# Kernel optimization log

Measured on AMD Instinct MI355X. Metric: run time of the kernel, lower is better.

Reference implementation:

```python
import jax, jax.numpy as jnp
import numpy as np

B, F = 512, 300  # F must satisfy F+4 == 16*19
EPS = 1e-5

def _leaky(v):
    return jnp.where(v >= 0, v, 0.01 * v)

def setup_inputs() -> dict:
    key = jax.random.key(0)
    ks = jax.random.split(key, 9)
    def conv_w(k, o, i):
        return jax.random.normal(k, (o, i), dtype=jnp.float32) * (1.0 / np.sqrt(i))
    x = jax.random.uniform(ks[0], (B, F), dtype=jnp.float32)
    return {
        "x": x,
        "w1": conv_w(ks[1], 256, 512), "b1": jnp.zeros((256,), jnp.float32),
        "w2": conv_w(ks[2], 128, 256), "b2": jnp.zeros((128,), jnp.float32),
        "w3": conv_w(ks[3], 64, 128),  "b3": jnp.zeros((64,), jnp.float32),
        "w4": conv_w(ks[4], 4, 64),    "b4": jnp.zeros((4,), jnp.float32),
    }

def reference(x, w1, b1, w2, b2, w3, b3, w4, b4):
    b = x.shape[0]
    xp = jnp.pad(x, ((0, 0), (2, 2)))                       # (b, 304)
    s1 = xp[:, None, :]                                      # unsqueeze(1)
    s2 = xp[:, :, None]                                      # unsqueeze(2)
    DI = s1 - s2                                             # (b,304,304)
    NDI = DI / (s1 + s2 + EPS)
    t = jnp.stack([DI, NDI], axis=-1)                        # (b,304,304,2)
    # tile into 16x16 grid of 19x19 patches, concat patches along channel
    # channel c = (row*16+col)*2 + d  (row-major loop order in original)
    t = t.reshape(b, 16, 19, 16, 19, 2).transpose(0, 2, 4, 1, 3, 5).reshape(b, 19, 19, 512)
    h = _leaky(jnp.einsum('bhwc,oc->bhwo', t, w1) + b1)      # (b,19,19,256)
    h = _leaky(jnp.einsum('bhwc,oc->bhwo', h, w2) + b2)      # (b,19,19,128)
    # masking branch (positional encoding in original is dead code / overwritten)
    m = jax.nn.relu(jnp.einsum('bhwc,oc->bhwo', h, w3) + b3)  # (b,19,19,64)
    m = jax.nn.relu(jnp.einsum('bhwc,oc->bhwo', m, w4) + b4)  # (b,19,19,4)
    m = m.transpose(3, 0, 1, 2).reshape(4, b, 19 * 19)
    m = jax.nn.softmax(m, axis=2).reshape(4, b, 19, 19, 1)
    # split 128 channels into 4 groups of 32
    g = h.reshape(b, 19, 19, 4, 32).transpose(3, 0, 1, 2, 4)  # (4,b,19,19,32)
    out = (g * m).sum(axis=(2, 3))                            # (4,b,32)
    return out.transpose(1, 0, 2).reshape(b, 128)
```

## Files before the change

### kernel.cpp

```cpp
#include <hip/hip_runtime.h>
#include <math.h>

typedef unsigned short ushort_t;
typedef __attribute__((ext_vector_type(8))) short short8;
typedef __attribute__((ext_vector_type(4))) float f32x4;

#define NTILES 12

#define WS_W_USHORTS 114688

__device__ inline ushort_t f2bf(float f) {
    unsigned u = __float_as_uint(f);
    return (ushort_t)((u + 0x7FFFu + ((u >> 16) & 1u)) >> 16);
}
__device__ inline unsigned pkbf(float f0, float f1) {
    unsigned a = __float_as_uint(f0) + 0x8000u;
    unsigned b = __float_as_uint(f1) + 0x8000u;
    return __builtin_amdgcn_perm(b, a, 0x07060302u);
}
__device__ inline float leaky(float v) { return fmaxf(v, 0.01f * v); }

__global__ void pack_weights(const float* __restrict__ w1, const float* __restrict__ w2,
                             const float* __restrict__ w3, ushort_t* __restrict__ ws) {
    const int idx = blockIdx.x * 256 + threadIdx.x;
    if (idx >= WS_W_USHORTS) return;
    float val = 0.f;
    if (idx < 73728) {
        const int j = idx & 7, lane = (idx >> 3) & 63, blk = idx >> 9;
        const int ks = blk % 9, os = blk / 9;
        const int m = lane & 15, q = lane >> 4;
        const int row = os * 16 + m;
        if (ks < 8) {
            const int k = ks * 32 + q * 8 + j;
            const int i1 = k >> 4, j1 = k & 15;
            val = w1[row * 512 + i1 * 32 + j1 * 2 + 1];
        } else {
            const int sub = q * 8 + j;
            if (sub < 16) {
                const int j1 = sub;
                float s = 0.f;
                #pragma unroll
                for (int i1 = 0; i1 < 16; ++i1) s += w1[row * 512 + i1 * 32 + j1 * 2];
                val = s;
            } else {
                const int i1 = sub - 16;
                float s = 0.f;
                #pragma unroll
                for (int j1 = 0; j1 < 16; ++j1) s += w1[row * 512 + i1 * 32 + j1 * 2];
                val = -s;
            }
        }
    } else if (idx < 106496) {
        const int l = idx - 73728;
        const int j = l & 7, lane = (l >> 3) & 63, blk = l >> 9;
        const int ks = blk & 7, os = blk >> 3;
        const int m = lane & 15, q = lane >> 4;
        val = w2[(os * 16 + m) * 256 + ks * 32 + q * 8 + j];
    } else {
        const int l = idx - 106496;
        const int j = l & 7, lane = (l >> 3) & 63, blk = l >> 9;
        const int ks = blk & 3, os = blk >> 2;
        const int m = lane & 15, q = lane >> 4;
        val = w3[(os * 16 + m) * 128 + ks * 32 + q * 8 + j];
    }
    ws[idx] = f2bf(val);
}

template <int NS>
__global__ __launch_bounds__(256, 3) void fused_mfma(
    const float* __restrict__ x, const ushort_t* __restrict__ ws,
    const float* __restrict__ b1, const float* __restrict__ b2,
    const float* __restrict__ b3, const float* __restrict__ b4,
    const float* __restrict__ w4,
    float* __restrict__ partA, float* __restrict__ partS)
{
    __shared__ __align__(16) ushort_t sm[19048];
    ushort_t* const ts   = sm;
    ushort_t* const h2s  = sm;
    ushort_t* const h1s  = sm + 10240;
    float*   const wbuf  = (float*)(sm + 10240);
    float*   const xp    = (float*)(sm + 18432);

    constexpr int SH  = (NS == 4) ? 2 : ((NS == 2) ? 1 : 0);
    constexpr int TPS = (NTILES + NS - 1) / NS;
    const int tid = threadIdx.x;
    const int s   = blockIdx.x & (NS - 1);
    const int bb  = blockIdx.x >> SH;
    const int t0  = s * TPS;
    const int t1  = (t0 + TPS < NTILES) ? (t0 + TPS) : NTILES;

    const int wid  = tid >> 6;
    const int lane = tid & 63;
    const int n0   = lane & 15;
    const int qi   = lane >> 4;
    const int sx   = n0 & 7;
    const int row0 = qi * 4;

    for (int jj = tid; jj < 308; jj += 256) {
        float v = 0.f;
        const int src = jj - 2;
        if (src >= 0 && src < 300) v = x[bb * 300 + src];
        xp[jj] = v;
    }

    const short8* wf1 = (const short8*)(ws);
    const short8* wf2 = (const short8*)(ws + 73728);
    const short8* wf3 = (const short8*)(ws + 106496);

    f32x4 bv1[4], bv2[2], bv3;
    #pragma unroll
    for (int jo = 0; jo < 4; ++jo) bv1[jo] = *(const f32x4*)&b1[(wid * 4 + jo) * 16 + row0];
    #pragma unroll
    for (int jo = 0; jo < 2; ++jo) bv2[jo] = *(const f32x4*)&b2[(wid * 2 + jo) * 16 + row0];
    bv3 = *(const f32x4*)&b3[wid * 16 + row0];
    short8 wr3[4];
    #pragma unroll
    for (int ks = 0; ks < 4; ++ks) wr3[ks] = wf3[(wid * 4 + ks) * 64 + lane];
    f32x4 w4r[4];
    #pragma unroll
    for (int q = 0; q < 4; ++q) w4r[q] = *(const f32x4*)&w4[q * 64 + wid * 16 + row0];
    const float b4s = b4[wid];

    f32x4 Afr[2] = {{0.f, 0.f, 0.f, 0.f}, {0.f, 0.f, 0.f, 0.f}};
    float Ss = 0.f;

    __syncthreads();

    for (int tile = t0; tile < t1; ++tile) {
        const int pos0 = tile * 32;

        {
            const int p   = tid & 31;
            const int i1b = tid >> 5;
            int posg = pos0 + p; if (posg > 360) posg = 360;
            const int hh = posg / 19;
            const int ww = posg - 19 * hh;
            const int base = p * 320;
            const int psw  = p & 7;
            float u[16];
            #pragma unroll
            for (int j1 = 0; j1 < 16; ++j1) u[j1] = xp[j1 * 19 + ww];
            #pragma unroll
            for (int ii = 0; ii < 2; ++ii) {
                const int i1 = i1b + ii * 8;
                const float v = xp[i1 * 19 + hh];
                #pragma unroll
                for (int j1 = 0; j1 < 16; j1 += 2) {
                    const float nd0 = (u[j1] - v)     * __builtin_amdgcn_rcpf(u[j1] + v + 1e-5f);
                    const float nd1 = (u[j1 + 1] - v) * __builtin_amdgcn_rcpf(u[j1 + 1] + v + 1e-5f);
                    const int oct = i1 * 2 + (j1 >> 3);
                    *(unsigned*)&ts[base + ((oct ^ psw) << 3) + (j1 & 7)] = pkbf(nd0, nd1);
                }
            }
            if (i1b == 0) {
                #pragma unroll
                for (int j1 = 0; j1 < 16; j1 += 2) {
                    const int oct = 32 + (j1 >> 3);
                    *(unsigned*)&ts[base + ((oct ^ psw) << 3) + (j1 & 7)] = pkbf(u[j1], u[j1 + 1]);
                }
                #pragma unroll
                for (int i1 = 0; i1 < 16; i1 += 2) {
                    const float v0 = xp[i1 * 19 + hh];
                    const float v1 = xp[(i1 + 1) * 19 + hh];
                    const int oct = 34 + (i1 >> 3);
                    *(unsigned*)&ts[base + ((oct ^ psw) << 3) + (i1 & 7)] = pkbf(v0, v1);
                }
            }
        }
        __syncthreads();

        {
            f32x4 acc[4][2];
            #pragma unroll
            for (int jo = 0; jo < 4; ++jo) { acc[jo][0] = bv1[jo]; acc[jo][1] = bv1[jo]; }
            const int tb0 = n0 * 320;
            const int tb1 = tb0 + 16 * 320;
            const int wbase = wid * 2304 + lane;
            #pragma unroll 3
            for (int ks = 0; ks < 9; ++ks) {
                const int oct = ks * 4 + qi;
                const short8 bb0 = *(const short8*)&ts[tb0 + ((oct ^ sx) << 3)];
                const short8 bb1 = *(const short8*)&ts[tb1 + ((oct ^ sx) << 3)];
                #pragma unroll
                for (int jo = 0; jo < 4; ++jo) {
                    const short8 a = wf1[wbase + (jo * 9 + ks) * 64];
                    acc[jo][0] = __builtin_amdgcn_mfma_f32_16x16x32_bf16(a, bb0, acc[jo][0], 0, 0, 0);
                    acc[jo][1] = __builtin_amdgcn_mfma_f32_16x16x32_bf16(a, bb1, acc[jo][1], 0, 0, 0);
                }
            }
            #pragma unroll
            for (int jo = 0; jo < 4; ++jo) {
                const int out0 = (wid * 4 + jo) * 16 + row0;
                #pragma unroll
                for (int ps = 0; ps < 2; ++ps) {
                    const f32x4 a4 = acc[jo][ps];
                    uint2 pk;
                    pk.x = pkbf(leaky(a4.x), leaky(a4.y));
                    pk.y = pkbf(leaky(a4.z), leaky(a4.w));
                    *(uint2*)&h1s[(ps * 16 + n0) * 256 + (((out0 >> 3) ^ sx) << 3) + (out0 & 7)] = pk;
                }
            }
        }
        __syncthreads();

        f32x4 h2f[2][2];
        {
            f32x4 acc[2][2];
            #pragma unroll
            for (int jo = 0; jo < 2; ++jo) { acc[jo][0] = bv2[jo]; acc[jo][1] = bv2[jo]; }
            const int hb0 = n0 * 256;
            const int hb1 = hb0 + 16 * 256;
            const int wbase = wid * 1024 + lane;
            #pragma unroll 4
            for (int ks = 0; ks < 8; ++ks) {
                const int oct = ks * 4 + qi;
                const short8 bb0 = *(const short8*)&h1s[hb0 + ((oct ^ sx) << 3)];
                const short8 bb1 = *(const short8*)&h1s[hb1 + ((oct ^ sx) << 3)];
                #pragma unroll
                for (int jo = 0; jo < 2; ++jo) {
                    const short8 a = wf2[wbase + (jo * 8 + ks) * 64];
                    acc[jo][0] = __builtin_amdgcn_mfma_f32_16x16x32_bf16(a, bb0, acc[jo][0], 0, 0, 0);
                    acc[jo][1] = __builtin_amdgcn_mfma_f32_16x16x32_bf16(a, bb1, acc[jo][1], 0, 0, 0);
                }
            }
            #pragma unroll
            for (int jo = 0; jo < 2; ++jo) {
                const int out0 = (wid * 2 + jo) * 16 + row0;
                #pragma unroll
                for (int ps = 0; ps < 2; ++ps) {
                    f32x4 a4 = acc[jo][ps];
                    a4.x = leaky(a4.x); a4.y = leaky(a4.y);
                    a4.z = leaky(a4.z); a4.w = leaky(a4.w);
                    h2f[jo][ps] = a4;
                    uint2 pk;
                    pk.x = pkbf(a4.x, a4.y);
                    pk.y = pkbf(a4.z, a4.w);
                    *(uint2*)&h2s[(ps * 16 + n0) * 128 + (((out0 >> 3) ^ sx) << 3) + (out0 & 7)] = pk;
                }
            }
        }
        __syncthreads();

        {
            f32x4 acc[2] = {bv3, bv3};
            const int cb0 = n0 * 128;
            const int cb1 = cb0 + 16 * 128;
            #pragma unroll
            for (int ks = 0; ks < 4; ++ks) {
                const int oct = ks * 4 + qi;
                const short8 bb0 = *(const short8*)&h2s[cb0 + ((oct ^ sx) << 3)];
                const short8 bb1 = *(const short8*)&h2s[cb1 + ((oct ^ sx) << 3)];
                acc[0] = __builtin_amdgcn_mfma_f32_16x16x32_bf16(wr3[ks], bb0, acc[0], 0, 0, 0);
                acc[1] = __builtin_amdgcn_mfma_f32_16x16x32_bf16(wr3[ks], bb1, acc[1], 0, 0, 0);
            }
            #pragma unroll
            for (int ps = 0; ps < 2; ++ps) {
                f32x4 m3 = acc[ps];
                m3.x = fmaxf(m3.x, 0.f); m3.y = fmaxf(m3.y, 0.f);
                m3.z = fmaxf(m3.z, 0.f); m3.w = fmaxf(m3.w, 0.f);
                float pl[4];
                #pragma unroll
                for (int q = 0; q < 4; ++q)
                    pl[q] = w4r[q].x * m3.x + w4r[q].y * m3.y + w4r[q].z * m3.z + w4r[q].w * m3.w;
                #pragma unroll
                for (int q = 0; q < 4; ++q) {
                    pl[q] += __shfl_xor(pl[q], 16, 64);
                    pl[q] += __shfl_xor(pl[q], 32, 64);
                }
                if (qi == 0) {
                    #pragma unroll
                    for (int q = 0; q < 4; ++q)
                        wbuf[(wid * 4 + q) * 32 + ps * 16 + n0] = pl[q];
                }
            }
        }
        __syncthreads();

        {
            #pragma unroll
            for (int ps = 0; ps < 2; ++ps) {
                const int pos = ps * 16 + n0;
                float lg = wbuf[(0 * 4 + wid) * 32 + pos] + wbuf[(1 * 4 + wid) * 32 + pos]
                         + wbuf[(2 * 4 + wid) * 32 + pos] + wbuf[(3 * 4 + wid) * 32 + pos] + b4s;
                lg = fmaxf(lg, 0.f);
                const float e = ((pos0 + pos) > 360) ? 0.f : __expf(lg);
                #pragma unroll
                for (int jo = 0; jo < 2; ++jo) {
                    Afr[jo].x += e * h2f[jo][ps].x;
                    Afr[jo].y += e * h2f[jo][ps].y;
                    Afr[jo].z += e * h2f[jo][ps].z;
                    Afr[jo].w += e * h2f[jo][ps].w;
                }
                Ss += e;
            }
        }
    }

    #pragma unroll
    for (int bit = 1; bit < 16; bit <<= 1) {
        #pragma unroll
        for (int jo = 0; jo < 2; ++jo) {
            Afr[jo].x += __shfl_xor(Afr[jo].x, bit, 64);
            Afr[jo].y += __shfl_xor(Afr[jo].y, bit, 64);
            Afr[jo].z += __shfl_xor(Afr[jo].z, bit, 64);
            Afr[jo].w += __shfl_xor(Afr[jo].w, bit, 64);
        }
        Ss += __shfl_xor(Ss, bit, 64);
    }
    if (n0 == 0) {
        const int pbA = (s * 512 + bb) * 128;
        #pragma unroll
        for (int jo = 0; jo < 2; ++jo) {
            const int ch0 = (wid * 2 + jo) * 16 + qi * 4;
            partA[pbA + ch0]     = Afr[jo].x;
            partA[pbA + ch0 + 1] = Afr[jo].y;
            partA[pbA + ch0 + 2] = Afr[jo].z;
            partA[pbA + ch0 + 3] = Afr[jo].w;
        }
        if (qi == 0) partS[(s * 512 + bb) * 4 + wid] = Ss;
    }
}

template <int NS>
__global__ void merge_out(const float* __restrict__ partA, const float* __restrict__ partS,
                          float* __restrict__ out) {
    const int idx = blockIdx.x * 256 + threadIdx.x;
    if (idx >= 512 * 128) return;
    const int bb = idx >> 7, ch = idx & 127;
    const int q = ch >> 5;
    float Sf = 0.f, Af = 0.f;
    #pragma unroll
    for (int s = 0; s < NS; ++s) {
        Af += partA[(s * 512 + bb) * 128 + ch];
        Sf += partS[(s * 512 + bb) * 4 + q];
    }
    out[idx] = Af / Sf;
}

__global__ __launch_bounds__(256, 2) void fallback_fused(
    const float* __restrict__ x,
    const float* __restrict__ w1, const float* __restrict__ b1,
    const float* __restrict__ w2, const float* __restrict__ b2,
    const float* __restrict__ w3, const float* __restrict__ b3,
    const float* __restrict__ w4, const float* __restrict__ b4,
    float* __restrict__ out)
{
    __shared__ float smf[14644];
    float* const xp  = smf;
    float* const ts  = smf + 308;
    float* const h1s = smf + 8500;
    float* const h2s = smf + 12596;
    float* const m3s = ts;
    float* const lgs = ts + 1024;

    const int tid = threadIdx.x;
    const int b   = blockIdx.x;
    for (int j = tid; j < 308; j += 256) {
        float v = 0.f;
        const int src = j - 2;
        if (src >= 0 && src < 300) v = x[b * 300 + src];
        xp[j] = v;
    }
    __syncthreads();
    const int q = tid >> 5, dd = tid & 31;
    float M = -1e30f, S = 0.f, A = 0.f;
    for (int tile = 0; tile < 23; ++tile) {
        const int pos0 = tile * 16;
        {
            const int p = tid & 15, kk0 = tid >> 4;
            const int pos = pos0 + p;
            const bool valid = (pos < 361);
            const int hh = valid ? (pos / 19) : 0;
            const int ww = valid ? (pos - hh * 19) : 0;
            #pragma unroll
            for (int i = 0; i < 16; ++i) {
                const int kk = kk0 + (i << 4);
                const int i1 = kk >> 4, j1 = kk & 15;
                float di = 0.f, ndi = 0.f;
                if (valid) {
                    const float u = xp[j1 * 19 + ww];
                    const float v = xp[i1 * 19 + hh];
                    di = u - v; ndi = di / (u + v + 1e-5f);
                }
                ts[(kk << 5) + p] = di;
                ts[(kk << 5) + 16 + p] = ndi;
            }
        }
        __syncthreads();
        {
            const int o = tid;
            float acc[16];
            const float bias = b1[o];
            #pragma unroll
            for (int p = 0; p < 16; ++p) acc[p] = bias;
            for (int k = 0; k < 512; ++k) {
                const float wv = w1[o * 512 + k];
                #pragma unroll
                for (int p = 0; p < 16; ++p) acc[p] += wv * ts[(k << 4) + p];
            }
            #pragma unroll
            for (int p = 0; p < 16; ++p) h1s[(o << 4) + p] = (acc[p] >= 0.f) ? acc[p] : 0.01f * acc[p];
        }
        __syncthreads();
        {
            const int o2 = tid & 127, pb = (tid >> 7) << 3;
            float acc[8];
            const float bias = b2[o2];
            #pragma unroll
            for (int j = 0; j < 8; ++j) acc[j] = bias;
            for (int k = 0; k < 256; ++k) {
                const float wv = w2[o2 * 256 + k];
                #pragma unroll
                for (int j = 0; j < 8; ++j) acc[j] += wv * h1s[(k << 4) + pb + j];
            }
            #pragma unroll
            for (int j = 0; j < 8; ++j) h2s[(o2 << 4) + pb + j] = (acc[j] >= 0.f) ? acc[j] : 0.01f * acc[j];
        }
        __syncthreads();
        {
            const int o3 = tid & 63, pb = (tid >> 6) << 2;
            float acc[4];
            const float bias = b3[o3];
            #pragma unroll
            for (int j = 0; j < 4; ++j) acc[j] = bias;
            for (int k = 0; k < 128; ++k) {
                const float wv = w3[o3 * 128 + k];
                #pragma unroll
                for (int j = 0; j < 4; ++j) acc[j] += wv * h2s[(k << 4) + pb + j];
            }
            #pragma unroll
            for (int j = 0; j < 4; ++j) m3s[(o3 << 4) + pb + j] = fmaxf(acc[j], 0.f);
        }
        __syncthreads();
        if (tid < 64) {
            const int o4 = tid >> 4, p = tid & 15;
            float a = b4[o4];
            for (int k = 0; k < 64; ++k) a += w4[o4 * 64 + k] * m3s[(k << 4) + p];
            a = fmaxf(a, 0.f);
            if (pos0 + p >= 361) a = -1e30f;
            lgs[(o4 << 4) + p] = a;
        }
        __syncthreads();
        if (tid < 128) {
            float l[16];
            #pragma unroll
            for (int p = 0; p < 16; ++p) l[p] = lgs[(q << 4) + p];
            float tmax = l[0];
            #pragma unroll
            for (int p = 1; p < 16; ++p) tmax = fmaxf(tmax, l[p]);
            const float newM = fmaxf(M, tmax);
            const float alpha = __expf(M - newM);
            float ssum = 0.f, asum = 0.f;
            #pragma unroll
            for (int p = 0; p < 16; ++p) {
                const float e = __expf(l[p] - newM);
                ssum += e;
                asum += e * h2s[(((q << 5) + dd) << 4) + p];
            }
            S = S * alpha + ssum; A = A * alpha + asum; M = newM;
        }
        __syncthreads();
    }
    if (tid < 128) out[(b << 7) + tid] = A / S;
}

extern "C" void kernel_launch(void* const* d_in, const int* in_sizes, int n_in,
                              void* d_out, int out_size, void* d_ws, size_t ws_size,
                              hipStream_t stream) {
    const float* x  = (const float*)d_in[0];
    const float* w1 = (const float*)d_in[1];
    const float* b1 = (const float*)d_in[2];
    const float* w2 = (const float*)d_in[3];
    const float* b2 = (const float*)d_in[4];
    const float* w3 = (const float*)d_in[5];
    const float* b3 = (const float*)d_in[6];
    const float* w4 = (const float*)d_in[7];
    const float* b4 = (const float*)d_in[8];
    float* out = (float*)d_out;

    const size_t wbytes = (size_t)WS_W_USHORTS * sizeof(ushort_t);
    ushort_t* ws = (ushort_t*)d_ws;
    const int packBlocks = (WS_W_USHORTS + 255) / 256;

    const size_t need4 = wbytes + (size_t)4 * 512 * 132 * sizeof(float);
    const size_t need2 = wbytes + (size_t)2 * 512 * 132 * sizeof(float);
    const size_t need1 = wbytes + (size_t)1 * 512 * 132 * sizeof(float);

    if (ws_size >= need4) {
        float* pA = (float*)((char*)d_ws + wbytes);
        float* pS = pA + (size_t)4 * 512 * 128;
        pack_weights<<<packBlocks, 256, 0, stream>>>(w1, w2, w3, ws);
        fused_mfma<4><<<2048, 256, 0, stream>>>(x, ws, b1, b2, b3, b4, w4, pA, pS);
        merge_out<4><<<256, 256, 0, stream>>>(pA, pS, out);
    } else if (ws_size >= need2) {
        float* pA = (float*)((char*)d_ws + wbytes);
        float* pS = pA + (size_t)2 * 512 * 128;
        pack_weights<<<packBlocks, 256, 0, stream>>>(w1, w2, w3, ws);
        fused_mfma<2><<<1024, 256, 0, stream>>>(x, ws, b1, b2, b3, b4, w4, pA, pS);
        merge_out<2><<<256, 256, 0, stream>>>(pA, pS, out);
    } else if (ws_size >= need1) {
        float* pA = (float*)((char*)d_ws + wbytes);
        float* pS = pA + (size_t)1 * 512 * 128;
        pack_weights<<<packBlocks, 256, 0, stream>>>(w1, w2, w3, ws);
        fused_mfma<1><<<512, 256, 0, stream>>>(x, ws, b1, b2, b3, b4, w4, pA, pS);
        merge_out<1><<<256, 256, 0, stream>>>(pA, pS, out);
    } else {
        fallback_fused<<<512, 256, 0, stream>>>(x, w1, b1, w2, b2, w3, b3, w4, b4, out);
    }
}
```

Baseline: 168.7 us.

## Switch layer-1/2 GEMMs to 32x32x16 MFMA with matching weight packing

Repacks w1 and w2 into the 32x32x16 bf16 MFMA fragment layout and rewrites the first two pointwise GEMMs to use 32x32 tiles. Each wave now handles one 32-position tile, which halves the LDS B-fragment reads per MFMA and changes the accumulator layout to 16 floats. The LDS swizzle changes to (n + n/8)&7 to avoid bank conflicts for 32-row access. The softmax accumulation and cross-lane reduction follow the new layout. Layer-3 weights and w4 now load inside the tile loop rather than being held in registers, which lowers register pressure but adds repeated global loads.

```diff
diff --git a/kernel.cpp b/kernel.cpp
--- a/kernel.cpp
+++ b/kernel.cpp
@@ -4,6 +4,7 @@
 typedef unsigned short ushort_t;
 typedef __attribute__((ext_vector_type(8))) short short8;
 typedef __attribute__((ext_vector_type(4))) float f32x4;
+typedef __attribute__((ext_vector_type(16))) float f32x16;
 
 #define NTILES 12
 
@@ -27,15 +28,15 @@
     float val = 0.f;
     if (idx < 73728) {
         const int j = idx & 7, lane = (idx >> 3) & 63, blk = idx >> 9;
-        const int ks = blk % 9, os = blk / 9;
-        const int m = lane & 15, q = lane >> 4;
-        const int row = os * 16 + m;
-        if (ks < 8) {
-            const int k = ks * 32 + q * 8 + j;
+        const int ks = blk % 18, os = blk / 18;
+        const int m = lane & 31, hf = lane >> 5;
+        const int row = os * 32 + m;
+        const int k = ks * 16 + hf * 8 + j;
+        if (k < 256) {
             const int i1 = k >> 4, j1 = k & 15;
             val = w1[row * 512 + i1 * 32 + j1 * 2 + 1];
         } else {
-            const int sub = q * 8 + j;
+            const int sub = k - 256;
             if (sub < 16) {
                 const int j1 = sub;
                 float s = 0.f;
@@ -53,9 +54,9 @@
     } else if (idx < 106496) {
         const int l = idx - 73728;
         const int j = l & 7, lane = (l >> 3) & 63, blk = l >> 9;
-        const int ks = blk & 7, os = blk >> 3;
-        const int m = lane & 15, q = lane >> 4;
-        val = w2[(os * 16 + m) * 256 + ks * 32 + q * 8 + j];
+        const int ks = blk & 15, os = blk >> 4;
+        const int m = lane & 31, hf = lane >> 5;
+        val = w2[(os * 32 + m) * 256 + ks * 16 + hf * 8 + j];
     } else {
         const int l = idx - 106496;
         const int j = l & 7, lane = (l >> 3) & 63, blk = l >> 9;
@@ -89,12 +90,16 @@
     const int t0  = s * TPS;
     const int t1  = (t0 + TPS < NTILES) ? (t0 + TPS) : NTILES;
 
-    const int wid  = tid >> 6;
-    const int lane = tid & 63;
-    const int n0   = lane & 15;
-    const int qi   = lane >> 4;
-    const int sx   = n0 & 7;
-    const int row0 = qi * 4;
+    const int wid   = tid >> 6;
+    const int lane  = tid & 63;
+    const int n     = lane & 31;
+    const int half5 = lane >> 5;
+    const int sxn   = (n + (n >> 3)) & 7;
+    const int n0  = lane & 15;
+    const int qi  = lane >> 4;
+    const int sxa = (n0 + (n0 >> 3)) & 7;
+    const int n0b = n0 + 16;
+    const int sxb = (n0b + (n0b >> 3)) & 7;
 
     for (int jj = tid; jj < 308; jj += 256) {
         float v = 0.f;
@@ -107,21 +112,26 @@
     const short8* wf2 = (const short8*)(ws + 73728);
     const short8* wf3 = (const short8*)(ws + 106496);
 
-    f32x4 bv1[4], bv2[2], bv3;
+    f32x16 bv1f[2], bv2f;
     #pragma unroll
-    for (int jo = 0; jo < 4; ++jo) bv1[jo] = *(const f32x4*)&b1[(wid * 4 + jo) * 16 + row0];
+    for (int jo = 0; jo < 2; ++jo) {
+        #pragma unroll
+        for (int g = 0; g < 4; ++g) {
+            const f32x4 t4 = *(const f32x4*)&b1[(wid * 2 + jo) * 32 + 8 * g + 4 * half5];
+            bv1f[jo][4 * g + 0] = t4.x; bv1f[jo][4 * g + 1] = t4.y;
+            bv1f[jo][4 * g + 2] = t4.z; bv1f[jo][4 * g + 3] = t4.w;
+        }
+    }
     #pragma unroll
-    for (int jo = 0; jo < 2; ++jo) bv2[jo] = *(const f32x4*)&b2[(wid * 2 + jo) * 16 + row0];
-    bv3 = *(const f32x4*)&b3[wid * 16 + row0];
-    short8 wr3[4];
-    #pragma unroll
-    for (int ks = 0; ks < 4; ++ks) wr3[ks] = wf3[(wid * 4 + ks) * 64 + lane];
-    f32x4 w4r[4];
-    #pragma unroll
-    for (int q = 0; q < 4; ++q) w4r[q] = *(const f32x4*)&w4[q * 64 + wid * 16 + row0];
+    for (int g = 0; g < 4; ++g) {
+        const f32x4 t4 = *(const f32x4*)&b2[wid * 32 + 8 * g + 4 * half5];
+        bv2f[4 * g + 0] = t4.x; bv2f[4 * g + 1] = t4.y;
+        bv2f[4 * g + 2] = t4.z; bv2f[4 * g + 3] = t4.w;
+    }
+    const f32x4 bv3 = *(const f32x4*)&b3[wid * 16 + qi * 4];
     const float b4s = b4[wid];
 
-    f32x4 Afr[2] = {{0.f, 0.f, 0.f, 0.f}, {0.f, 0.f, 0.f, 0.f}};
+    f32x16 Afr = {0.f};
     float Ss = 0.f;
 
     __syncthreads();
@@ -136,7 +146,7 @@
             const int hh = posg / 19;
             const int ww = posg - 19 * hh;
             const int base = p * 320;
-            const int psw  = p & 7;
+            const int sxp  = (p + (p >> 3)) & 7;
             float u[16];
             #pragma unroll
             for (int j1 = 0; j1 < 16; ++j1) u[j1] = xp[j1 * 19 + ww];
@@ -149,113 +159,96 @@
                     const float nd0 = (u[j1] - v)     * __builtin_amdgcn_rcpf(u[j1] + v + 1e-5f);
                     const float nd1 = (u[j1 + 1] - v) * __builtin_amdgcn_rcpf(u[j1 + 1] + v + 1e-5f);
                     const int oct = i1 * 2 + (j1 >> 3);
-                    *(unsigned*)&ts[base + ((oct ^ psw) << 3) + (j1 & 7)] = pkbf(nd0, nd1);
+                    *(unsigned*)&ts[base + ((oct ^ sxp) << 3) + (j1 & 7)] = pkbf(nd0, nd1);
                 }
             }
             if (i1b == 0) {
                 #pragma unroll
                 for (int j1 = 0; j1 < 16; j1 += 2) {
                     const int oct = 32 + (j1 >> 3);
-                    *(unsigned*)&ts[base + ((oct ^ psw) << 3) + (j1 & 7)] = pkbf(u[j1], u[j1 + 1]);
+                    *(unsigned*)&ts[base + ((oct ^ sxp) << 3) + (j1 & 7)] = pkbf(u[j1], u[j1 + 1]);
                 }
                 #pragma unroll
                 for (int i1 = 0; i1 < 16; i1 += 2) {
                     const float v0 = xp[i1 * 19 + hh];
                     const float v1 = xp[(i1 + 1) * 19 + hh];
                     const int oct = 34 + (i1 >> 3);
-                    *(unsigned*)&ts[base + ((oct ^ psw) << 3) + (i1 & 7)] = pkbf(v0, v1);
-                }
-            }
-        }
-        __syncthreads();
-
-        {
-            f32x4 acc[4][2];
-            #pragma unroll
-            for (int jo = 0; jo < 4; ++jo) { acc[jo][0] = bv1[jo]; acc[jo][1] = bv1[jo]; }
-            const int tb0 = n0 * 320;
-            const int tb1 = tb0 + 16 * 320;
-            const int wbase = wid * 2304 + lane;
-            #pragma unroll 3
-            for (int ks = 0; ks < 9; ++ks) {
-                const int oct = ks * 4 + qi;
-                const short8 bb0 = *(const short8*)&ts[tb0 + ((oct ^ sx) << 3)];
-                const short8 bb1 = *(const short8*)&ts[tb1 + ((oct ^ sx) << 3)];
-                #pragma unroll
-                for (int jo = 0; jo < 4; ++jo) {
-                    const short8 a = wf1[wbase + (jo * 9 + ks) * 64];
-                    acc[jo][0] = __builtin_amdgcn_mfma_f32_16x16x32_bf16(a, bb0, acc[jo][0], 0, 0, 0);
-                    acc[jo][1] = __builtin_amdgcn_mfma_f32_16x16x32_bf16(a, bb1, acc[jo][1], 0, 0, 0);
-                }
-            }
-            #pragma unroll
-            for (int jo = 0; jo < 4; ++jo) {
-                const int out0 = (wid * 4 + jo) * 16 + row0;
-                #pragma unroll
-                for (int ps = 0; ps < 2; ++ps) {
-                    const f32x4 a4 = acc[jo][ps];
+                    *(unsigned*)&ts[base + ((oct ^ sxp) << 3) + (i1 & 7)] = pkbf(v0, v1);
+                }
+            }
+        }
+        __syncthreads();
+
+        {
+            f32x16 acc[2] = {bv1f[0], bv1f[1]};
+            const int tb = n * 320;
+            #pragma unroll 6
+            for (int ks = 0; ks < 18; ++ks) {
+                const int oct = ks * 2 + half5;
+                const short8 bbv = *(const short8*)&ts[tb + ((oct ^ sxn) << 3)];
+                acc[0] = __builtin_amdgcn_mfma_f32_32x32x16_bf16(
+                    wf1[((wid * 2 + 0) * 18 + ks) * 64 + lane], bbv, acc[0], 0, 0, 0);
+                acc[1] = __builtin_amdgcn_mfma_f32_32x32x16_bf16(
+                    wf1[((wid * 2 + 1) * 18 + ks) * 64 + lane], bbv, acc[1], 0, 0, 0);
+            }
+            #pragma unroll
+            for (int jo = 0; jo < 2; ++jo) {
+                const int osb = (wid * 2 + jo) * 32;
+                #pragma unroll
+                for (int g = 0; g < 4; ++g) {
                     uint2 pk;
-                    pk.x = pkbf(leaky(a4.x), leaky(a4.y));
-                    pk.y = pkbf(leaky(a4.z), leaky(a4.w));
-                    *(uint2*)&h1s[(ps * 16 + n0) * 256 + (((out0 >> 3) ^ sx) << 3) + (out0 & 7)] = pk;
-                }
-            }
-        }
-        __syncthreads();
-
-        f32x4 h2f[2][2];
-        {
-            f32x4 acc[2][2];
-            #pragma unroll
-            for (int jo = 0; jo < 2; ++jo) { acc[jo][0] = bv2[jo]; acc[jo][1] = bv2[jo]; }
-            const int hb0 = n0 * 256;
-            const int hb1 = hb0 + 16 * 256;
-            const int wbase = wid * 1024 + lane;
-            #pragma unroll 4
-            for (int ks = 0; ks < 8; ++ks) {
-                const int oct = ks * 4 + qi;
-                const short8 bb0 = *(const short8*)&h1s[hb0 + ((oct ^ sx) << 3)];
-                const short8 bb1 = *(const short8*)&h1s[hb1 + ((oct ^ sx) << 3)];
-                #pragma unroll
-                for (int jo = 0; jo < 2; ++jo) {
-                    const short8 a = wf2[wbase + (jo * 8 + ks) * 64];
-                    acc[jo][0] = __builtin_amdgcn_mfma_f32_16x16x32_bf16(a, bb0, acc[jo][0], 0, 0, 0);
-                    acc[jo][1] = __builtin_amdgcn_mfma_f32_16x16x32_bf16(a, bb1, acc[jo][1], 0, 0, 0);
-                }
-            }
-            #pragma unroll
-            for (int jo = 0; jo < 2; ++jo) {
-                const int out0 = (wid * 2 + jo) * 16 + row0;
-                #pragma unroll
-                for (int ps = 0; ps < 2; ++ps) {
-                    f32x4 a4 = acc[jo][ps];
-                    a4.x = leaky(a4.x); a4.y = leaky(a4.y);
-                    a4.z = leaky(a4.z); a4.w = leaky(a4.w);
-                    h2f[jo][ps] = a4;
-                    uint2 pk;
-                    pk.x = pkbf(a4.x, a4.y);
-                    pk.y = pkbf(a4.z, a4.w);
-                    *(uint2*)&h2s[(ps * 16 + n0) * 128 + (((out0 >> 3) ^ sx) << 3) + (out0 & 7)] = pk;
-                }
-            }
-        }
-        __syncthreads();
-
-        {
-            f32x4 acc[2] = {bv3, bv3};
+                    pk.x = pkbf(leaky(acc[jo][4 * g + 0]), leaky(acc[jo][4 * g + 1]));
+                    pk.y = pkbf(leaky(acc[jo][4 * g + 2]), leaky(acc[jo][4 * g + 3]));
+                    const int ch0 = osb + 8 * g + 4 * half5;
+                    *(uint2*)&h1s[n * 256 + (((ch0 >> 3) ^ sxn) << 3) + (ch0 & 7)] = pk;
+                }
+            }
+        }
+        __syncthreads();
+
+        f32x16 h2v;
+        {
+            f32x16 acc = bv2f;
+            const int hb = n * 256;
+            #pragma unroll 8
+            for (int ks = 0; ks < 16; ++ks) {
+                const int oct = ks * 2 + half5;
+                const short8 bbv = *(const short8*)&h1s[hb + ((oct ^ sxn) << 3)];
+                acc = __builtin_amdgcn_mfma_f32_32x32x16_bf16(
+                    wf2[(wid * 16 + ks) * 64 + lane], bbv, acc, 0, 0, 0);
+            }
+            #pragma unroll
+            for (int r = 0; r < 16; ++r) h2v[r] = leaky(acc[r]);
+            #pragma unroll
+            for (int g = 0; g < 4; ++g) {
+                uint2 pk;
+                pk.x = pkbf(h2v[4 * g + 0], h2v[4 * g + 1]);
+                pk.y = pkbf(h2v[4 * g + 2], h2v[4 * g + 3]);
+                const int ch0 = wid * 32 + 8 * g + 4 * half5;
+                *(uint2*)&h2s[n * 128 + (((ch0 >> 3) ^ sxn) << 3) + (ch0 & 7)] = pk;
+            }
+        }
+        __syncthreads();
+
+        {
+            f32x4 acc3[2] = {bv3, bv3};
             const int cb0 = n0 * 128;
-            const int cb1 = cb0 + 16 * 128;
+            const int cb1 = n0b * 128;
             #pragma unroll
             for (int ks = 0; ks < 4; ++ks) {
                 const int oct = ks * 4 + qi;
-                const short8 bb0 = *(const short8*)&h2s[cb0 + ((oct ^ sx) << 3)];
-                const short8 bb1 = *(const short8*)&h2s[cb1 + ((oct ^ sx) << 3)];
-                acc[0] = __builtin_amdgcn_mfma_f32_16x16x32_bf16(wr3[ks], bb0, acc[0], 0, 0, 0);
-                acc[1] = __builtin_amdgcn_mfma_f32_16x16x32_bf16(wr3[ks], bb1, acc[1], 0, 0, 0);
-            }
+                const short8 bb0 = *(const short8*)&h2s[cb0 + ((oct ^ sxa) << 3)];
+                const short8 bb1 = *(const short8*)&h2s[cb1 + ((oct ^ sxb) << 3)];
+                const short8 a = wf3[(wid * 4 + ks) * 64 + lane];
+                acc3[0] = __builtin_amdgcn_mfma_f32_16x16x32_bf16(a, bb0, acc3[0], 0, 0, 0);
+                acc3[1] = __builtin_amdgcn_mfma_f32_16x16x32_bf16(a, bb1, acc3[1], 0, 0, 0);
+            }
+            f32x4 w4r[4];
+            #pragma unroll
+            for (int q = 0; q < 4; ++q) w4r[q] = *(const f32x4*)&w4[q * 64 + wid * 16 + qi * 4];
             #pragma unroll
             for (int ps = 0; ps < 2; ++ps) {
-                f32x4 m3 = acc[ps];
+                f32x4 m3 = acc3[ps];
                 m3.x = fmaxf(m3.x, 0.f); m3.y = fmaxf(m3.y, 0.f);
                 m3.z = fmaxf(m3.z, 0.f); m3.w = fmaxf(m3.w, 0.f);
                 float pl[4];
@@ -277,47 +270,32 @@
         __syncthreads();
 
         {
-            #pragma unroll
-            for (int ps = 0; ps < 2; ++ps) {
-                const int pos = ps * 16 + n0;
-                float lg = wbuf[(0 * 4 + wid) * 32 + pos] + wbuf[(1 * 4 + wid) * 32 + pos]
-                         + wbuf[(2 * 4 + wid) * 32 + pos] + wbuf[(3 * 4 + wid) * 32 + pos] + b4s;
-                lg = fmaxf(lg, 0.f);
-                const float e = ((pos0 + pos) > 360) ? 0.f : __expf(lg);
-                #pragma unroll
-                for (int jo = 0; jo < 2; ++jo) {
-                    Afr[jo].x += e * h2f[jo][ps].x;
-                    Afr[jo].y += e * h2f[jo][ps].y;
-                    Afr[jo].z += e * h2f[jo][ps].z;
-                    Afr[jo].w += e * h2f[jo][ps].w;
-                }
-                Ss += e;
-            }
+            float lg = wbuf[(0 * 4 + wid) * 32 + n] + wbuf[(1 * 4 + wid) * 32 + n]
+                     + wbuf[(2 * 4 + wid) * 32 + n] + wbuf[(3 * 4 + wid) * 32 + n] + b4s;
+            lg = fmaxf(lg, 0.f);
+            const float e = ((pos0 + n) > 360) ? 0.f : __expf(lg);
+            #pragma unroll
+            for (int r = 0; r < 16; ++r) Afr[r] += e * h2v[r];
+            Ss += e;
         }
     }
 
     #pragma unroll
-    for (int bit = 1; bit < 16; bit <<= 1) {
+    for (int bit = 1; bit < 32; bit <<= 1) {
         #pragma unroll
-        for (int jo = 0; jo < 2; ++jo) {
-            Afr[jo].x += __shfl_xor(Afr[jo].x, bit, 64);
-            Afr[jo].y += __shfl_xor(Afr[jo].y, bit, 64);
-            Afr[jo].z += __shfl_xor(Afr[jo].z, bit, 64);
-            Afr[jo].w += __shfl_xor(Afr[jo].w, bit, 64);
-        }
+        for (int r = 0; r < 16; ++r) Afr[r] += __shfl_xor(Afr[r], bit, 64);
         Ss += __shfl_xor(Ss, bit, 64);
     }
-    if (n0 == 0) {
-        const int pbA = (s * 512 + bb) * 128;
+    if (n == 0) {
+        const int pbA = (s * 512 + bb) * 128 + wid * 32 + 4 * half5;
         #pragma unroll
-        for (int jo = 0; jo < 2; ++jo) {
-            const int ch0 = (wid * 2 + jo) * 16 + qi * 4;
-            partA[pbA + ch0]     = Afr[jo].x;
-            partA[pbA + ch0 + 1] = Afr[jo].y;
-            partA[pbA + ch0 + 2] = Afr[jo].z;
-            partA[pbA + ch0 + 3] = Afr[jo].w;
-        }
-        if (qi == 0) partS[(s * 512 + bb) * 4 + wid] = Ss;
+        for (int g = 0; g < 4; ++g) {
+            f32x4 o4;
+            o4.x = Afr[4 * g + 0]; o4.y = Afr[4 * g + 1];
+            o4.z = Afr[4 * g + 2]; o4.w = Afr[4 * g + 3];
+            *(f32x4*)&partA[pbA + 8 * g] = o4;
+        }
+        if (half5 == 0) partS[(s * 512 + bb) * 4 + wid] = Ss;
     }
 }
 
```

New measurement: 208.7 us. +23.7%, slower.

## Split fused MFMA block work across 8 waves instead of 4

Applied to the files above, without the earlier changes.

The fused kernel now launches 512-thread blocks, so each of 8 waves computes half as many output rows in layers 1 and 2. Layer 3 work is split across output slices and position halves, and the w3/w4 register preloads become per-use global loads. The aim is more waves per CU to hide MFMA and global-load latency and to cut per-wave register pressure. In exchange, the per-block reductions are restructured, w4/w3 are reloaded every tile, and the occupancy limit rises to launch_bounds(512,4), which may force register spills.

```diff
diff --git a/kernel.cpp b/kernel.cpp
--- a/kernel.cpp
+++ b/kernel.cpp
@@ -67,7 +67,7 @@
 }
 
 template <int NS>
-__global__ __launch_bounds__(256, 3) void fused_mfma(
+__global__ __launch_bounds__(512, 4) void fused_mfma(
     const float* __restrict__ x, const ushort_t* __restrict__ ws,
     const float* __restrict__ b1, const float* __restrict__ b2,
     const float* __restrict__ b3, const float* __restrict__ b4,
@@ -89,14 +89,17 @@
     const int t0  = s * TPS;
     const int t1  = (t0 + TPS < NTILES) ? (t0 + TPS) : NTILES;
 
-    const int wid  = tid >> 6;
+    const int wv   = tid >> 6;
     const int lane = tid & 63;
     const int n0   = lane & 15;
     const int qi   = lane >> 4;
     const int sx   = n0 & 7;
     const int row0 = qi * 4;
-
-    for (int jj = tid; jj < 308; jj += 256) {
+    const int o3s  = wv & 3;
+    const int ps3  = wv >> 2;
+    const int qh   = wv >> 1;
+
+    for (int jj = tid; jj < 308; jj += 512) {
         float v = 0.f;
         const int src = jj - 2;
         if (src >= 0 && src < 300) v = x[bb * 300 + src];
@@ -107,19 +110,12 @@
     const short8* wf2 = (const short8*)(ws + 73728);
     const short8* wf3 = (const short8*)(ws + 106496);
 
-    f32x4 bv1[4], bv2[2], bv3;
+    f32x4 bv1[2], bv2, bv3;
     #pragma unroll
-    for (int jo = 0; jo < 4; ++jo) bv1[jo] = *(const f32x4*)&b1[(wid * 4 + jo) * 16 + row0];
-    #pragma unroll
-    for (int jo = 0; jo < 2; ++jo) bv2[jo] = *(const f32x4*)&b2[(wid * 2 + jo) * 16 + row0];
-    bv3 = *(const f32x4*)&b3[wid * 16 + row0];
-    short8 wr3[4];
-    #pragma unroll
-    for (int ks = 0; ks < 4; ++ks) wr3[ks] = wf3[(wid * 4 + ks) * 64 + lane];
-    f32x4 w4r[4];
-    #pragma unroll
-    for (int q = 0; q < 4; ++q) w4r[q] = *(const f32x4*)&w4[q * 64 + wid * 16 + row0];
-    const float b4s = b4[wid];
+    for (int jo = 0; jo < 2; ++jo) bv1[jo] = *(const f32x4*)&b1[(wv * 2 + jo) * 16 + row0];
+    bv2 = *(const f32x4*)&b2[wv * 16 + row0];
+    bv3 = *(const f32x4*)&b3[o3s * 16 + row0];
+    const float b4s = b4[qh];
 
     f32x4 Afr[2] = {{0.f, 0.f, 0.f, 0.f}, {0.f, 0.f, 0.f, 0.f}};
     float Ss = 0.f;
@@ -130,67 +126,64 @@
         const int pos0 = tile * 32;
 
         {
-            const int p   = tid & 31;
-            const int i1b = tid >> 5;
+            const int p  = tid & 31;
+            const int i1 = tid >> 5;
             int posg = pos0 + p; if (posg > 360) posg = 360;
             const int hh = posg / 19;
             const int ww = posg - 19 * hh;
             const int base = p * 320;
             const int psw  = p & 7;
+            const float v = xp[i1 * 19 + hh];
             float u[16];
             #pragma unroll
             for (int j1 = 0; j1 < 16; ++j1) u[j1] = xp[j1 * 19 + ww];
             #pragma unroll
-            for (int ii = 0; ii < 2; ++ii) {
-                const int i1 = i1b + ii * 8;
-                const float v = xp[i1 * 19 + hh];
-                #pragma unroll
-                for (int j1 = 0; j1 < 16; j1 += 2) {
-                    const float nd0 = (u[j1] - v)     * __builtin_amdgcn_rcpf(u[j1] + v + 1e-5f);
-                    const float nd1 = (u[j1 + 1] - v) * __builtin_amdgcn_rcpf(u[j1 + 1] + v + 1e-5f);
-                    const int oct = i1 * 2 + (j1 >> 3);
-                    *(unsigned*)&ts[base + ((oct ^ psw) << 3) + (j1 & 7)] = pkbf(nd0, nd1);
-                }
-            }
-            if (i1b == 0) {
+            for (int j1 = 0; j1 < 16; j1 += 2) {
+                const float nd0 = (u[j1] - v)     * __builtin_amdgcn_rcpf(u[j1] + v + 1e-5f);
+                const float nd1 = (u[j1 + 1] - v) * __builtin_amdgcn_rcpf(u[j1 + 1] + v + 1e-5f);
+                const int oct = i1 * 2 + (j1 >> 3);
+                *(unsigned*)&ts[base + ((oct ^ psw) << 3) + (j1 & 7)] = pkbf(nd0, nd1);
+            }
+            if (i1 == 0) {
                 #pragma unroll
                 for (int j1 = 0; j1 < 16; j1 += 2) {
                     const int oct = 32 + (j1 >> 3);
                     *(unsigned*)&ts[base + ((oct ^ psw) << 3) + (j1 & 7)] = pkbf(u[j1], u[j1 + 1]);
                 }
-                #pragma unroll
-                for (int i1 = 0; i1 < 16; i1 += 2) {
-                    const float v0 = xp[i1 * 19 + hh];
-                    const float v1 = xp[(i1 + 1) * 19 + hh];
-                    const int oct = 34 + (i1 >> 3);
-                    *(unsigned*)&ts[base + ((oct ^ psw) << 3) + (i1 & 7)] = pkbf(v0, v1);
+            } else if (i1 == 1) {
+                #pragma unroll
+                for (int i2 = 0; i2 < 16; i2 += 2) {
+                    const float v0 = xp[i2 * 19 + hh];
+                    const float v1 = xp[(i2 + 1) * 19 + hh];
+                    const int oct = 34 + (i2 >> 3);
+                    *(unsigned*)&ts[base + ((oct ^ psw) << 3) + (i2 & 7)] = pkbf(v0, v1);
                 }
             }
         }
         __syncthreads();
 
         {
-            f32x4 acc[4][2];
-            #pragma unroll
-            for (int jo = 0; jo < 4; ++jo) { acc[jo][0] = bv1[jo]; acc[jo][1] = bv1[jo]; }
+            f32x4 acc[2][2];
+            #pragma unroll
+            for (int jo = 0; jo < 2; ++jo) { acc[jo][0] = bv1[jo]; acc[jo][1] = bv1[jo]; }
             const int tb0 = n0 * 320;
             const int tb1 = tb0 + 16 * 320;
-            const int wbase = wid * 2304 + lane;
+            const int wbase = wv * 1152 + lane;
             #pragma unroll 3
             for (int ks = 0; ks < 9; ++ks) {
                 const int oct = ks * 4 + qi;
                 const short8 bb0 = *(const short8*)&ts[tb0 + ((oct ^ sx) << 3)];
                 const short8 bb1 = *(const short8*)&ts[tb1 + ((oct ^ sx) << 3)];
                 #pragma unroll
-                for (int jo = 0; jo < 4; ++jo) {
+                for (int jo = 0; jo < 2; ++jo) {
                     const short8 a = wf1[wbase + (jo * 9 + ks) * 64];
                     acc[jo][0] = __builtin_amdgcn_mfma_f32_16x16x32_bf16(a, bb0, acc[jo][0], 0, 0, 0);
                     acc[jo][1] = __builtin_amdgcn_mfma_f32_16x16x32_bf16(a, bb1, acc[jo][1], 0, 0, 0);
                 }
             }
             #pragma unroll
-            for (int jo = 0; jo < 4; ++jo) {
-                const int out0 = (wid * 4 + jo) * 16 + row0;
+            for (int jo = 0; jo < 2; ++jo) {
+                const int out0 = (wv * 2 + jo) * 16 + row0;
                 #pragma unroll
                 for (int ps = 0; ps < 2; ++ps) {
                     const f32x4 a4 = acc[jo][ps];
@@ -203,75 +196,63 @@
         }
         __syncthreads();
 
-        f32x4 h2f[2][2];
-        {
-            f32x4 acc[2][2];
-            #pragma unroll
-            for (int jo = 0; jo < 2; ++jo) { acc[jo][0] = bv2[jo]; acc[jo][1] = bv2[jo]; }
+        f32x4 h2f[2];
+        {
+            f32x4 acc[2] = {bv2, bv2};
             const int hb0 = n0 * 256;
             const int hb1 = hb0 + 16 * 256;
-            const int wbase = wid * 1024 + lane;
             #pragma unroll 4
             for (int ks = 0; ks < 8; ++ks) {
                 const int oct = ks * 4 + qi;
                 const short8 bb0 = *(const short8*)&h1s[hb0 + ((oct ^ sx) << 3)];
                 const short8 bb1 = *(const short8*)&h1s[hb1 + ((oct ^ sx) << 3)];
-                #pragma unroll
-                for (int jo = 0; jo < 2; ++jo) {
-                    const short8 a = wf2[wbase + (jo * 8 + ks) * 64];
-                    acc[jo][0] = __builtin_amdgcn_mfma_f32_16x16x32_bf16(a, bb0, acc[jo][0], 0, 0, 0);
-                    acc[jo][1] = __builtin_amdgcn_mfma_f32_16x16x32_bf16(a, bb1, acc[jo][1], 0, 0, 0);
-                }
-            }
-            #pragma unroll
-            for (int jo = 0; jo < 2; ++jo) {
-                const int out0 = (wid * 2 + jo) * 16 + row0;
-                #pragma unroll
-                for (int ps = 0; ps < 2; ++ps) {
-                    f32x4 a4 = acc[jo][ps];
-                    a4.x = leaky(a4.x); a4.y = leaky(a4.y);
-                    a4.z = leaky(a4.z); a4.w = leaky(a4.w);
-                    h2f[jo][ps] = a4;
-                    uint2 pk;
-                    pk.x = pkbf(a4.x, a4.y);
-                    pk.y = pkbf(a4.z, a4.w);
-                    *(uint2*)&h2s[(ps * 16 + n0) * 128 + (((out0 >> 3) ^ sx) << 3) + (out0 & 7)] = pk;
-                }
-            }
-        }
-        __syncthreads();
-
-        {
-            f32x4 acc[2] = {bv3, bv3};
-            const int cb0 = n0 * 128;
-            const int cb1 = cb0 + 16 * 128;
+                const short8 a = wf2[(wv * 8 + ks) * 64 + lane];
+                acc[0] = __builtin_amdgcn_mfma_f32_16x16x32_bf16(a, bb0, acc[0], 0, 0, 0);
+                acc[1] = __builtin_amdgcn_mfma_f32_16x16x32_bf16(a, bb1, acc[1], 0, 0, 0);
+            }
+            const int out0 = wv * 16 + row0;
+            #pragma unroll
+            for (int ps = 0; ps < 2; ++ps) {
+                f32x4 a4 = acc[ps];
+                a4.x = leaky(a4.x); a4.y = leaky(a4.y);
+                a4.z = leaky(a4.z); a4.w = leaky(a4.w);
+                h2f[ps] = a4;
+                uint2 pk;
+                pk.x = pkbf(a4.x, a4.y);
+                pk.y = pkbf(a4.z, a4.w);
+                *(uint2*)&h2s[(ps * 16 + n0) * 128 + (((out0 >> 3) ^ sx) << 3) + (out0 & 7)] = pk;
+            }
+        }
+        __syncthreads();
+
+        {
+            f32x4 acc = bv3;
+            const int cb = (ps3 * 16 + n0) * 128;
             #pragma unroll
             for (int ks = 0; ks < 4; ++ks) {
                 const int oct = ks * 4 + qi;
-                const short8 bb0 = *(const short8*)&h2s[cb0 + ((oct ^ sx) << 3)];
-                const short8 bb1 = *(const short8*)&h2s[cb1 + ((oct ^ sx) << 3)];
-                acc[0] = __builtin_amdgcn_mfma_f32_16x16x32_bf16(wr3[ks], bb0, acc[0], 0, 0, 0);
-                acc[1] = __builtin_amdgcn_mfma_f32_16x16x32_bf16(wr3[ks], bb1, acc[1], 0, 0, 0);
-            }
-            #pragma unroll
-            for (int ps = 0; ps < 2; ++ps) {
-                f32x4 m3 = acc[ps];
-                m3.x = fmaxf(m3.x, 0.f); m3.y = fmaxf(m3.y, 0.f);
-                m3.z = fmaxf(m3.z, 0.f); m3.w = fmaxf(m3.w, 0.f);
-                float pl[4];
+                const short8 bbv = *(const short8*)&h2s[cb + ((oct ^ sx) << 3)];
+                const short8 a = wf3[(o3s * 4 + ks) * 64 + lane];
+                acc = __builtin_amdgcn_mfma_f32_16x16x32_bf16(a, bbv, acc, 0, 0, 0);
+            }
+            f32x4 m3 = acc;
+            m3.x = fmaxf(m3.x, 0.f); m3.y = fmaxf(m3.y, 0.f);
+            m3.z = fmaxf(m3.z, 0.f); m3.w = fmaxf(m3.w, 0.f);
+            float pl[4];
+            #pragma unroll
+            for (int q = 0; q < 4; ++q) {
+                const f32x4 w4r = *(const f32x4*)&w4[q * 64 + o3s * 16 + row0];
+                pl[q] = w4r.x * m3.x + w4r.y * m3.y + w4r.z * m3.z + w4r.w * m3.w;
+            }
+            #pragma unroll
+            for (int q = 0; q < 4; ++q) {
+                pl[q] += __shfl_xor(pl[q], 16, 64);
+                pl[q] += __shfl_xor(pl[q], 32, 64);
+            }
+            if (qi == 0) {
                 #pragma unroll
                 for (int q = 0; q < 4; ++q)
-                    pl[q] = w4r[q].x * m3.x + w4r[q].y * m3.y + w4r[q].z * m3.z + w4r[q].w * m3.w;
-                #pragma unroll
-                for (int q = 0; q < 4; ++q) {
-                    pl[q] += __shfl_xor(pl[q], 16, 64);
-                    pl[q] += __shfl_xor(pl[q], 32, 64);
-                }
-                if (qi == 0) {
-                    #pragma unroll
-                    for (int q = 0; q < 4; ++q)
-                        wbuf[(wid * 4 + q) * 32 + ps * 16 + n0] = pl[q];
-                }
+                    wbuf[(o3s * 4 + q) * 32 + ps3 * 16 + n0] = pl[q];
             }
         }
         __syncthreads();
@@ -280,44 +261,37 @@
             #pragma unroll
             for (int ps = 0; ps < 2; ++ps) {
                 const int pos = ps * 16 + n0;
-                float lg = wbuf[(0 * 4 + wid) * 32 + pos] + wbuf[(1 * 4 + wid) * 32 + pos]
-                         + wbuf[(2 * 4 + wid) * 32 + pos] + wbuf[(3 * 4 + wid) * 32 + pos] + b4s;
+                float lg = wbuf[(0 * 4 + qh) * 32 + pos] + wbuf[(1 * 4 + qh) * 32 + pos]
+                         + wbuf[(2 * 4 + qh) * 32 + pos] + wbuf[(3 * 4 + qh) * 32 + pos] + b4s;
                 lg = fmaxf(lg, 0.f);
                 const float e = ((pos0 + pos) > 360) ? 0.f : __expf(lg);
-                #pragma unroll
-                for (int jo = 0; jo < 2; ++jo) {
-                    Afr[jo].x += e * h2f[jo][ps].x;
-                    Afr[jo].y += e * h2f[jo][ps].y;
-                    Afr[jo].z += e * h2f[jo][ps].z;
-                    Afr[jo].w += e * h2f[jo][ps].w;
-                }
+                Afr[ps].x += e * h2f[ps].x;
+                Afr[ps].y += e * h2f[ps].y;
+                Afr[ps].z += e * h2f[ps].z;
+                Afr[ps].w += e * h2f[ps].w;
                 Ss += e;
             }
         }
     }
 
+    f32x4 At;
+    At.x = Afr[0].x + Afr[1].x; At.y = Afr[0].y + Afr[1].y;
+    At.z = Afr[0].z + Afr[1].z; At.w = Afr[0].w + Afr[1].w;
     #pragma unroll
     for (int bit = 1; bit < 16; bit <<= 1) {
-        #pragma unroll
-        for (int jo = 0; jo < 2; ++jo) {
-            Afr[jo].x += __shfl_xor(Afr[jo].x, bit, 64);
-            Afr[jo].y += __shfl_xor(Afr[jo].y, bit, 64);
-            Afr[jo].z += __shfl_xor(Afr[jo].z, bit, 64);
-            Afr[jo].w += __shfl_xor(Afr[jo].w, bit, 64);
-        }
+        At.x += __shfl_xor(At.x, bit, 64);
+        At.y += __shfl_xor(At.y, bit, 64);
+        At.z += __shfl_xor(At.z, bit, 64);
+        At.w += __shfl_xor(At.w, bit, 64);
         Ss += __shfl_xor(Ss, bit, 64);
     }
     if (n0 == 0) {
-        const int pbA = (s * 512 + bb) * 128;
-        #pragma unroll
-        for (int jo = 0; jo < 2; ++jo) {
-            const int ch0 = (wid * 2 + jo) * 16 + qi * 4;
-            partA[pbA + ch0]     = Afr[jo].x;
-            partA[pbA + ch0 + 1] = Afr[jo].y;
-            partA[pbA + ch0 + 2] = Afr[jo].z;
-            partA[pbA + ch0 + 3] = Afr[jo].w;
-        }
-        if (qi == 0) partS[(s * 512 + bb) * 4 + wid] = Ss;
+        const int pbA = (s * 512 + bb) * 128 + wv * 16 + row0;
+        partA[pbA]     = At.x;
+        partA[pbA + 1] = At.y;
+        partA[pbA + 2] = At.z;
+        partA[pbA + 3] = At.w;
+        if (qi == 0 && (wv & 1) == 0) partS[(s * 512 + bb) * 4 + qh] = Ss;
     }
 }
 
@@ -490,19 +464,19 @@
         float* pA = (float*)((char*)d_ws + wbytes);
         float* pS = pA + (size_t)4 * 512 * 128;
         pack_weights<<<packBlocks, 256, 0, stream>>>(w1, w2, w3, ws);
-        fused_mfma<4><<<2048, 256, 0, stream>>>(x, ws, b1, b2, b3, b4, w4, pA, pS);
+        fused_mfma<4><<<2048, 512, 0, stream>>>(x, ws, b1, b2, b3, b4, w4, pA, pS);
         merge_out<4><<<256, 256, 0, stream>>>(pA, pS, out);
     } else if (ws_size >= need2) {
         float* pA = (float*)((char*)d_ws + wbytes);
         float* pS = pA + (size_t)2 * 512 * 128;
         pack_weights<<<packBlocks, 256, 0, stream>>>(w1, w2, w3, ws);
-        fused_mfma<2><<<1024, 256, 0, stream>>>(x, ws, b1, b2, b3, b4, w4, pA, pS);
+        fused_mfma<2><<<1024, 512, 0, stream>>>(x, ws, b1, b2, b3, b4, w4, pA, pS);
         merge_out<2><<<256, 256, 0, stream>>>(pA, pS, out);
     } else if (ws_size >= need1) {
         float* pA = (float*)((char*)d_ws + wbytes);
         float* pS = pA + (size_t)1 * 512 * 128;
         pack_weights<<<packBlocks, 256, 0, stream>>>(w1, w2, w3, ws);
-        fused_mfma<1><<<512, 256, 0, stream>>>(x, ws, b1, b2, b3, b4, w4, pA, pS);
+        fused_mfma<1><<<512, 512, 0, stream>>>(x, ws, b1, b2, b3, b4, w4, pA, pS);
         merge_out<1><<<256, 256, 0, stream>>>(pA, pS, out);
     } else {
         fallback_fused<<<512, 256, 0, stream>>>(x, w1, b1, w2, b2, w3, b3, w4, b4, out);
```

Result: faster. 150.4 us (-10.9%).
